# Optimization experiments

Hardware: AMD Instinct MI355X
Metric: run time of the kernel (lower is better)

## Reference

```python
import jax, jax.numpy as jnp
import numpy as np

B, T, C, H, S = 4, 1024, 768, 12, 64  # batch, seq, emb_dim, n_heads, head_size
FF = 4 * C          # 3072, ff_hidden_size (required by SwiGLU input dim)
HID = int(8 * C / 3)  # 2048, SwiGLU hidden
EPS = 1e-6


def _rope_tables(seq_len, dim):
    # theta = 10000 ** (-2 * arange(0, dim, 2) / dim)  (note extra factor 2 vs standard RoPE)
    theta = 10000.0 ** (-2.0 * jnp.arange(0, dim, 2, dtype=jnp.float32) / dim)
    freqs = jnp.arange(seq_len, dtype=jnp.float32)[:, None] * theta  # [T, dim/2]
    cos = jnp.repeat(jnp.cos(freqs), 2, axis=-1)  # [T, dim]
    sin = jnp.repeat(jnp.sin(freqs), 2, axis=-1)
    return cos, sin


def _rope(x, cos, sin):
    # x: [..., T, S]; rotate pairs: even' = -odd, odd' = even
    rot = jnp.stack([-x[..., 1::2], x[..., 0::2]], axis=-1).reshape(x.shape)
    return x * cos + rot * sin


def _rmsnorm(x, gamma):
    # global scalar RMS over the whole tensor (faithful to torch.mean with no dim)
    return x / jnp.sqrt(EPS + jnp.mean(x * x)) * gamma


def _block(x, Wq, Wk, Wv, Wo, g1, g2, W1, b1, Ww, bw, Wg, bg, Wd, bd, W2, b2):
    Tlen = x.shape[1]
    cos, sin = _rope_tables(Tlen, S)
    # --- multi-head attention on rms1(x) ---
    h = _rmsnorm(x, g1)
    q = jnp.einsum('btc,hcs->bhts', h, Wq)
    k = jnp.einsum('btc,hcs->bhts', h, Wk)
    v = jnp.einsum('btc,hcs->bhts', h, Wv)
    rq = _rope(q, cos, sin)
    rk = _rope(k, cos, sin)
    scores = jnp.einsum('bhts,bhks->bhtk', rq, rk) * (C ** -0.5)  # scale by emb_dim, faithful
    causal = jnp.tril(jnp.ones((Tlen, Tlen), dtype=bool))
    scores = jnp.where(causal, scores, -jnp.inf)
    probs = jax.nn.softmax(scores, axis=-1)
    attn = jnp.einsum('bhtk,bhks->bhts', probs, v)
    attn = attn.transpose(0, 2, 1, 3).reshape(x.shape[0], Tlen, C)  # concat heads
    out = x + attn @ Wo
    # --- feed forward on rms2(out) ---
    h2 = _rmsnorm(out, g2)
    u = h2 @ W1 + b1                      # [B,T,FF]
    wx = u @ Ww + bw                      # [B,T,HID]
    vx = u @ Wg + bg
    ff = (wx * (vx * jax.nn.sigmoid(vx))) @ Wd + bd  # [B,T,FF]
    ff = ff @ W2 + b2                     # [B,T,C]
    return out + ff


def setup_inputs() -> dict:
    key = jax.random.key(0)
    ks = jax.random.split(key, 17)
    sd = 0.02
    return {
        'x':  jax.random.normal(ks[0], (B, T, C), jnp.float32),
        'Wq': jax.random.normal(ks[1], (H, C, S), jnp.float32) * sd,
        'Wk': jax.random.normal(ks[2], (H, C, S), jnp.float32) * sd,
        'Wv': jax.random.normal(ks[3], (H, C, S), jnp.float32) * sd,
        'Wo': jax.random.normal(ks[4], (C, C), jnp.float32) * sd,
        'g1': jnp.ones((C,), jnp.float32),
        'g2': jnp.ones((C,), jnp.float32),
        'W1': jax.random.normal(ks[5], (C, FF), jnp.float32) * sd,
        'b1': jnp.zeros((FF,), jnp.float32),
        'Ww': jax.random.normal(ks[6], (FF, HID), jnp.float32) * sd,
        'bw': jnp.zeros((HID,), jnp.float32),
        'Wg': jax.random.normal(ks[7], (FF, HID), jnp.float32) * sd,
        'bg': jnp.zeros((HID,), jnp.float32),
        'Wd': jax.random.normal(ks[8], (HID, FF), jnp.float32) * sd,
        'bd': jnp.zeros((FF,), jnp.float32),
        'W2': jax.random.normal(ks[9], (FF, C), jnp.float32) * sd,
        'b2': jnp.zeros((C,), jnp.float32),
    }


def reference(x, Wq, Wk, Wv, Wo, g1, g2, W1, b1, Ww, bw, Wg, bg, Wd, bd, W2, b2):
    return _block(x, Wq, Wk, Wv, Wo, g1, g2, W1, b1, Ww, bw, Wg, bg, Wd, bd, W2, b2)
```

## Files before the change

kernel.cpp:

```cpp
#include <hip/hip_runtime.h>
#include <math.h>

#define BB   4
#define TT   1024
#define CC   768
#define HH   12
#define SS   64
#define FFD  3072
#define HIDD 2048
#define NTOK (BB*TT)
#define EPSR 1e-6f

typedef __attribute__((ext_vector_type(8))) short bf16x8;
typedef __attribute__((ext_vector_type(4))) float f32x4;

__device__ __forceinline__ unsigned short f2bf(float f) {
    unsigned u = __float_as_uint(f);
    return (unsigned short)((u + 0x7FFFu + ((u >> 16) & 1u)) >> 16);
}
__device__ __forceinline__ float bfl(unsigned u) { return __uint_as_float(u << 16); }
__device__ __forceinline__ float bfh(unsigned u) { return __uint_as_float(u & 0xFFFF0000u); }
__device__ __forceinline__ unsigned pk2(float a, float b) {
    return (unsigned)f2bf(a) | ((unsigned)f2bf(b) << 16);
}

__device__ __forceinline__ void gload_lds16(const unsigned short* g, unsigned short* l) {
    __builtin_amdgcn_global_load_lds(
        (const __attribute__((address_space(1))) unsigned int*)g,
        (__attribute__((address_space(3))) unsigned int*)l, 16, 0, 0);
}

__global__ void k_scale_gamma_b(const float* __restrict__ x, const float* __restrict__ g,
                                const float* __restrict__ part, unsigned short* __restrict__ h,
                                int n8, float invn, int npart) {
    __shared__ float sm[256];
    float s = 0.f;
    for (int i = threadIdx.x; i < npart; i += 256) s += part[i];
    sm[threadIdx.x] = s;
    __syncthreads();
    for (int off = 128; off > 0; off >>= 1) {
        if (threadIdx.x < off) sm[threadIdx.x] += sm[threadIdx.x + off];
        __syncthreads();
    }
    float sc = 1.0f / sqrtf(EPSR + sm[0] * invn);
    int i = blockIdx.x * blockDim.x + threadIdx.x;
    if (i >= n8) return;
    float4 v0 = ((const float4*)x)[2*i];
    float4 v1 = ((const float4*)x)[2*i+1];
    int c = (i * 8) % CC;
    float4 g0 = *(const float4*)(g + c);
    float4 g1v = *(const float4*)(g + c + 4);
    uint4 r;
    r.x = pk2(v0.x*sc*g0.x,  v0.y*sc*g0.y);
    r.y = pk2(v0.z*sc*g0.z,  v0.w*sc*g0.w);
    r.z = pk2(v1.x*sc*g1v.x, v1.y*sc*g1v.y);
    r.w = pk2(v1.z*sc*g1v.z, v1.w*sc*g1v.w);
    ((uint4*)h)[i] = r;
}

#define TQKV 1728
#define TWO  576
#define TW1  2304
#define TWW  6144
#define TWD  6144
#define TW2  2304
#define J0 (TQKV)
#define J1 (J0 + TWO)
#define J2 (J1 + TW1)
#define J3 (J2 + TWW)
#define J4 (J3 + TWW)
#define J5 (J4 + TWD)
#define J6 (J5 + TW2)
#define J7 (J6 + 16)
#define J8 (J7 + 128)
#define JSUM 1024
#define J9 (J8 + JSUM)

__device__ __forceinline__ void wT_tile(float (*tl)[33], const float* __restrict__ W,
                                        unsigned short* __restrict__ Wt,
                                        int K, int N, int t, int tx, int ty) {
    int nk = K >> 5;
    int k0 = (t % nk) * 32, n0 = (t / nk) * 32;
#pragma unroll
    for (int i = 0; i < 4; ++i)
        tl[ty + i*8][tx] = W[(size_t)(k0 + ty + i*8) * N + n0 + tx];
    __syncthreads();
#pragma unroll
    for (int i = 0; i < 4; ++i)
        Wt[(size_t)(n0 + ty + i*8) * K + k0 + tx] = f2bf(tl[tx][ty + i*8]);
}

__device__ __forceinline__ void wT_tile_il(float (*tl)[33], const float* __restrict__ W,
                                           unsigned short* __restrict__ Wt,
                                           int K, int N, int t, int tx, int ty, int ofs) {
    int nk = K >> 5;
    int k0 = (t % nk) * 32, n0 = (t / nk) * 32;
#pragma unroll
    for (int i = 0; i < 4; ++i)
        tl[ty + i*8][tx] = W[(size_t)(k0 + ty + i*8) * N + n0 + tx];
    __syncthreads();
#pragma unroll
    for (int i = 0; i < 4; ++i) {
        int j = n0 + ty + i*8;
        int pr = ((j & ~15) << 1) + ofs*16 + (j & 15);
        Wt[(size_t)pr * K + k0 + tx] = f2bf(tl[tx][ty + i*8]);
    }
}

__global__ void k_prep(const float* __restrict__ Wq, const float* __restrict__ Wk,
                       const float* __restrict__ Wv, const float* __restrict__ Wo,
                       const float* __restrict__ W1, const float* __restrict__ Ww,
                       const float* __restrict__ Wg, const float* __restrict__ Wd,
                       const float* __restrict__ W2, const float* __restrict__ bw,
                       const float* __restrict__ bg, const float* __restrict__ x,
                       unsigned short* __restrict__ wqkvT, unsigned short* __restrict__ WoT,
                       unsigned short* __restrict__ W1T, unsigned short* __restrict__ WcatT,
                       unsigned short* __restrict__ WdT, unsigned short* __restrict__ W2T,
                       float* __restrict__ bcat, float* __restrict__ tab,
                       float* __restrict__ part) {
    __shared__ float tl[32][33];
    const int bid = blockIdx.x;
    const int tx = threadIdx.x & 31, ty = threadIdx.x >> 5;
    if (bid < J0) {
        int t = bid;
        int c0 = (t % 24) * 32;
        int s0 = ((t / 24) & 1) * 32;
        int z = t / 48, sel = z / HH, h = z % HH;
        const float* W = (sel == 0 ? Wq : (sel == 1 ? Wk : Wv)) + (size_t)h * CC * SS;
#pragma unroll
        for (int i = 0; i < 4; ++i)
            tl[ty + i*8][tx] = W[(size_t)(c0 + ty + i*8) * SS + s0 + tx];
        __syncthreads();
#pragma unroll
        for (int i = 0; i < 4; ++i)
            wqkvT[(size_t)(sel*CC + h*SS + s0 + ty + i*8) * CC + c0 + tx] = f2bf(tl[tx][ty + i*8]);
    } else if (bid < J1) {
        wT_tile(tl, Wo, WoT, CC, CC, bid - J0, tx, ty);
    } else if (bid < J2) {
        wT_tile(tl, W1, W1T, CC, FFD, bid - J1, tx, ty);
    } else if (bid < J3) {
        wT_tile_il(tl, Ww, WcatT, FFD, HIDD, bid - J2, tx, ty, 0);
    } else if (bid < J4) {
        wT_tile_il(tl, Wg, WcatT, FFD, HIDD, bid - J3, tx, ty, 1);
    } else if (bid < J5) {
        wT_tile(tl, Wd, WdT, HIDD, FFD, bid - J4, tx, ty);
    } else if (bid < J6) {
        wT_tile(tl, W2, W2T, FFD, CC, bid - J5, tx, ty);
    } else if (bid < J7) {
        int ip = (bid - J6) * 256 + threadIdx.x;
        int lg = ((ip >> 5) << 4) + (ip & 15);
        bcat[ip] = ((ip >> 4) & 1) ? bg[lg] : bw[lg];
    } else if (bid < J8) {
        int i = (bid - J7) * 256 + threadIdx.x;
        int t = i >> 5, j = i & 31;
        float th = expf(-(float)j * 0.5756462732485115f);
        float ang = (float)t * th;
        tab[2*i]   = cosf(ang);
        tab[2*i+1] = sinf(ang);
    } else {
        float* sm = &tl[0][0];
        const int pb = bid - J8;
        const int n4 = NTOK * CC / 4;
        float s = 0.f;
        int stride = JSUM * 256;
        for (int i = pb * 256 + threadIdx.x; i < n4; i += stride) {
            float4 v = ((const float4*)x)[i];
            s += v.x*v.x + v.y*v.y + v.z*v.z + v.w*v.w;
        }
        sm[threadIdx.x] = s;
        __syncthreads();
        for (int off = 128; off > 0; off >>= 1) {
            if (threadIdx.x < off) sm[threadIdx.x] += sm[threadIdx.x + off];
            __syncthreads();
        }
        if (threadIdx.x == 0) part[pb] = sm[0];
    }
}

__global__ void k_rope_vt(unsigned short* __restrict__ qkv, const float* __restrict__ tab,
                          unsigned short* __restrict__ vtg) {
    const int bid = blockIdx.x;
    if (bid < 6144) {
        int i = bid * 256 + threadIdx.x;
        int j  = i & 31;
        int h  = (i >> 5) % HH;
        int bt = i / (32 * HH);
        int t  = bt & (TT - 1);
        float cs = tab[(t*32 + j)*2];
        float sn = tab[(t*32 + j)*2 + 1];
        size_t base = (size_t)bt * (3*CC) + h * SS + 2*j;
        unsigned q = *(unsigned*)(qkv + base);
        float qe = bfl(q), qo = bfh(q);
        *(unsigned*)(qkv + base) = pk2(qe*cs - qo*sn, qo*cs + qe*sn);
        unsigned k = *(unsigned*)(qkv + base + CC);
        float ke = bfl(k), ko = bfh(k);
        *(unsigned*)(qkv + base + CC) = pk2(ke*cs - ko*sn, ko*cs + ke*sn);
    } else {
        int b2 = bid - 6144;
        int bh = b2 >> 3, ty = b2 & 7;
        int b = bh / HH, h = bh % HH;
        int d = threadIdx.x & 63, tq = threadIdx.x >> 6;
        int t0 = ty * 128 + tq * 32;
        const unsigned short* src = qkv + (size_t)(b*TT + t0)*(3*CC) + 2*CC + h*SS + d;
        unsigned v[16];
#pragma unroll
        for (int e = 0; e < 16; ++e) {
            unsigned lo = src[(size_t)(2*e)*(3*CC)];
            unsigned hi = src[(size_t)(2*e+1)*(3*CC)];
            v[e] = (lo & 0xFFFFu) | (hi << 16);
        }
        uint4* dst = (uint4*)(vtg + ((size_t)bh*64 + d)*TT + t0);
#pragma unroll
        for (int q = 0; q < 4; ++q)
            dst[q] = make_uint4(v[q*4], v[q*4+1], v[q*4+2], v[q*4+3]);
    }
}

template<bool BIAS, bool RES, bool OUTB, bool SSQ>
__global__ __launch_bounds__(256) void k_gemm_bf16(
    const unsigned short* __restrict__ A, const unsigned short* __restrict__ Bt,
    const float* __restrict__ bias, const float* __restrict__ res,
    void* __restrict__ Cv, int M, int N, int K, float* __restrict__ ssq_part)
{
    __shared__ unsigned short As[2][128*32];
    __shared__ unsigned short Bs[2][128*32];
    __shared__ float smr[256];
    const int tid  = threadIdx.x;
    const int w    = tid >> 6, lane = tid & 63;
    const int wr   = w >> 1,  wc   = w & 1;
    const int row0 = blockIdx.y * 128, col0 = blockIdx.x * 128;

    f32x4 acc[4][4];
#pragma unroll
    for (int m = 0; m < 4; ++m)
#pragma unroll
        for (int n = 0; n < 4; ++n) acc[m][n] = (f32x4){0.f, 0.f, 0.f, 0.f};

    const int lr4 = lane >> 2;
    const int scb = lane & 3;

    auto stage = [&](int t, int buf) {
#pragma unroll
        for (int i = 0; i < 2; ++i) {
            int lr = w * 32 + i * 16 + lr4;
            int cbs = scb ^ ((lr >> 1) & 3);
            const unsigned short* ga = A + (size_t)(row0 + lr) * K + t * 32 + cbs * 8;
            gload_lds16(ga, &As[buf][(w * 32 + i * 16) * 32]);
            const unsigned short* gb = Bt + (size_t)(col0 + lr) * K + t * 32 + cbs * 8;
            gload_lds16(gb, &Bs[buf][(w * 32 + i * 16) * 32]);
        }
    };

    const int nt = K / 32;
    stage(0, 0);
    int cur = 0;
    const int fr = lane & 15, fq = lane >> 4;
    for (int t = 0; t < nt; ++t) {
        __syncthreads();
        if (t + 1 < nt) stage(t + 1, cur ^ 1);
        bf16x8 af[4], bf[4];
#pragma unroll
        for (int m = 0; m < 4; ++m) {
            int ra = wr * 64 + m * 16 + fr;
            af[m] = *(const bf16x8*)&As[cur][ra * 32 + (fq ^ ((ra >> 1) & 3)) * 8];
            int rb = wc * 64 + m * 16 + fr;
            bf[m] = *(const bf16x8*)&Bs[cur][rb * 32 + (fq ^ ((rb >> 1) & 3)) * 8];
        }
#pragma unroll
        for (int m = 0; m < 4; ++m)
#pragma unroll
            for (int n = 0; n < 4; ++n)
                acc[m][n] = __builtin_amdgcn_mfma_f32_16x16x32_bf16(af[m], bf[n], acc[m][n], 0, 0, 0);
        cur ^= 1;
    }

    float ssq = 0.f;
#pragma unroll
    for (int m = 0; m < 4; ++m) {
#pragma unroll
        for (int n = 0; n < 4; ++n) {
            int col = col0 + wc * 64 + n * 16 + fr;
            float bv = BIAS ? bias[col] : 0.f;
#pragma unroll
            for (int j = 0; j < 4; ++j) {
                int row = row0 + wr * 64 + m * 16 + fq * 4 + j;
                size_t off = (size_t)row * N + col;
                float v = acc[m][n][j] + bv;
                if (RES) v += res[off];
                if (OUTB) ((unsigned short*)Cv)[off] = f2bf(v);
                else      ((float*)Cv)[off] = v;
                if (SSQ) ssq += v * v;
            }
        }
    }
    if (SSQ) {
        smr[tid] = ssq;
        __syncthreads();
        for (int off = 128; off > 0; off >>= 1) {
            if (tid < off) smr[tid] += smr[tid + off];
            __syncthreads();
        }
        if (tid == 0) ssq_part[blockIdx.y * gridDim.x + blockIdx.x] = smr[0];
    }
}

#define GSTEP(s_, DOSTAGE, GATE)                                                  \
    {                                                                             \
        const int st_ = (s_) & 3;                                                 \
        const unsigned short* pa_ = &ringA[st_][0];                               \
        const unsigned short* pb_ = &ringB[st_][0];                               \
        bf16x8 af[8], bv[4];                                                      \
        _Pragma("unroll")                                                         \
        for (int m = 0; m < 8; ++m)                                               \
            af[m] = *(const bf16x8*)&pa_[offA[m]];                                \
        _Pragma("unroll")                                                         \
        for (int n = 0; n < 4; ++n)                                               \
            bv[n] = *(const bf16x8*)&pb_[offB[n]];                                \
        if (DOSTAGE) { stageA((s_) + 3); stageB((s_) + 3); }                      \
        __builtin_amdgcn_sched_barrier(0);                                        \
        __builtin_amdgcn_s_setprio(1);                                            \
        _Pragma("unroll")                                                         \
        for (int m = 0; m < 8; ++m)                                               \
            _Pragma("unroll")                                                     \
            for (int n = 0; n < 4; ++n)                                           \
                acc[m][n] = __builtin_amdgcn_mfma_f32_16x16x32_bf16(              \
                    af[m], bv[n], acc[m][n], 0, 0, 0);                            \
        __builtin_amdgcn_s_setprio(0);                                            \
        asm volatile("s_waitcnt " GATE ::: "memory");                             \
        __builtin_amdgcn_sched_barrier(0);                                        \
        __builtin_amdgcn_s_barrier();                                             \
    }

template<bool BIAS, bool SWIGLU>
__global__ __launch_bounds__(512, 2) void k_gemm256(
    const unsigned short* __restrict__ A, const unsigned short* __restrict__ Bt,
    const float* __restrict__ bias, unsigned short* __restrict__ C,
    int M, int N, int K)
{
    __shared__ __align__(16) unsigned short ringA[4][256*32];
    __shared__ __align__(16) unsigned short ringB[4][256*32];
    const int tid = threadIdx.x;
    const int w = tid >> 6, lane = tid & 63;
    const int wm = w >> 2, wn = w & 3;
    const int fr = lane & 15, fq = lane >> 4;

    const int nwg = gridDim.x * gridDim.y;
    const int bid = blockIdx.y * gridDim.x + blockIdx.x;
    const int cpx = nwg >> 3;
    const int sbid = (bid & 7) * cpx + (bid >> 3);
    const int row0 = (sbid / gridDim.x) * 256;
    const int col0 = (sbid % gridDim.x) * 256;

    f32x4 acc[8][4];
#pragma unroll
    for (int m = 0; m < 8; ++m)
#pragma unroll
        for (int n = 0; n < 4; ++n) acc[m][n] = (f32x4){0.f, 0.f, 0.f, 0.f};

    const int c0 = tid, c1 = 512 + tid;
    const int r0 = c0 >> 2, p0 = ((c0 & 3) ^ ((r0 >> 1) & 3)) * 8;
    const int r1 = c1 >> 2, p1 = ((c1 & 3) ^ ((r1 >> 1) & 3)) * 8;
    const unsigned short* aS0 = A  + (size_t)(row0 + r0) * K + p0;
    const unsigned short* aS1 = A  + (size_t)(row0 + r1) * K + p1;
    const unsigned short* bS0 = Bt + (size_t)(col0 + r0) * K + p0;
    const unsigned short* bS1 = Bt + (size_t)(col0 + r1) * K + p1;
    const int dL = w * 512;
    auto stageA = [&](int t) {
        const int st = t & 3;
        const int kb = t * 32;
        gload_lds16(aS0 + kb, &ringA[st][dL]);
        gload_lds16(aS1 + kb, &ringA[st][4096 + dL]);
    };
    auto stageB = [&](int t) {
        const int st = t & 3;
        const int kb = t * 32;
        gload_lds16(bS0 + kb, &ringB[st][dL]);
        gload_lds16(bS1 + kb, &ringB[st][4096 + dL]);
    };

    int offA[8], offB[4];
#pragma unroll
    for (int m = 0; m < 8; ++m) {
        int ra = wm*128 + m*16 + fr;
        offA[m] = ra*32 + (fq ^ ((ra >> 1) & 3))*8;
    }
#pragma unroll
    for (int n = 0; n < 4; ++n) {
        int rb = wn*64 + n*16 + fr;
        offB[n] = rb*32 + (fq ^ ((rb >> 1) & 3))*8;
    }

    const int S = K >> 5;
    stageA(0); stageB(0); stageA(1); stageB(1); stageA(2); stageB(2);
    asm volatile("s_waitcnt vmcnt(8)" ::: "memory");
    __builtin_amdgcn_s_barrier();
    int s = 0;
    for (; s < S - 3; ++s) GSTEP(s, true, "vmcnt(8)");
    GSTEP(s, false, "vmcnt(4)"); ++s;
    GSTEP(s, false, "vmcnt(0)"); ++s;
    GSTEP(s, false, "vmcnt(0)");

    if (SWIGLU) {
#pragma unroll
        for (int m = 0; m < 8; ++m) {
#pragma unroll
            for (int n = 0; n < 4; n += 2) {
                int colw = col0 + wn*64 + n*16 + fr;
                float bw_ = BIAS ? bias[colw] : 0.f;
                float bg_ = BIAS ? bias[colw + 16] : 0.f;
                int colo = ((colw >> 5) << 4) + (colw & 15);
#pragma unroll
                for (int j = 0; j < 4; ++j) {
                    int row = row0 + wm*128 + m*16 + fq*4 + j;
                    float wx = acc[m][n][j] + bw_;
                    float vx = acc[m][n+1][j] + bg_;
                    float sw = wx * vx / (1.f + __expf(-vx));
                    C[(size_t)row * (N >> 1) + colo] = f2bf(sw);
                }
            }
        }
    } else {
#pragma unroll
        for (int m = 0; m < 8; ++m) {
#pragma unroll
            for (int n = 0; n < 4; ++n) {
                int col = col0 + wn*64 + n*16 + fr;
                float bvb = BIAS ? bias[col] : 0.f;
#pragma unroll
                for (int j = 0; j < 4; ++j) {
                    int row = row0 + wm*128 + m*16 + fq*4 + j;
                    C[(size_t)row * N + col] = f2bf(acc[m][n][j] + bvb);
                }
            }
        }
    }
}

__global__ __launch_bounds__(256) void k_attn_mfma(
    const unsigned short* __restrict__ qkv, const unsigned short* __restrict__ vtg,
    unsigned short* __restrict__ attn)
{
    __shared__ __align__(16) unsigned short Ks[2][64*64];
    __shared__ __align__(16) unsigned short Vs[2][64*64];
    __shared__ __align__(16) unsigned short Ps[4][16*72];
    const int tid = threadIdx.x;
    const int w = tid >> 6, lane = tid & 63;
    const int fr = lane & 15, fq = lane >> 4;
    const int bh = blockIdx.x, b = bh / HH, h = bh % HH;
    const int qb = blockIdx.y * 64;
    const int nkt = qb / 64 + 1;
    const float scale = 0.03608439182435161f;

    bf16x8 qf[2];
    {
        const unsigned short* qp = qkv + (size_t)(b*TT + qb + w*16 + fr)*(3*CC) + h*SS + fq*8;
        qf[0] = *(const bf16x8*)qp;
        qf[1] = *(const bf16x8*)(qp + 32);
    }

    auto stage = [&](int kt, int buf) {
        const unsigned short* kbase = qkv + (size_t)(b*TT + kt*64)*(3*CC) + CC + h*SS;
        const unsigned short* vbase = vtg + ((size_t)bh*64)*TT + kt*64;
#pragma unroll
        for (int p = 0; p < 2; ++p) {
            int s = p*256 + tid;
            int row = s >> 3;
            int blk = (s & 7) ^ (row & 7);
            gload_lds16(kbase + (size_t)row*(3*CC) + blk*8, &Ks[buf][(p*256 + w*64)*8]);
            gload_lds16(vbase + (size_t)row*TT + blk*8,     &Vs[buf][(p*256 + w*64)*8]);
        }
    };

    float m[4] = {-INFINITY, -INFINITY, -INFINITY, -INFINITY};
    float l[4] = {0.f, 0.f, 0.f, 0.f};
    f32x4 oacc[4];
#pragma unroll
    for (int n = 0; n < 4; ++n) oacc[n] = (f32x4){0.f, 0.f, 0.f, 0.f};

    stage(0, 0);
    int cur = 0;
    for (int kt = 0; kt < nkt; ++kt) {
        __syncthreads();
        if (kt + 1 < nkt) stage(kt + 1, cur ^ 1);

        f32x4 sacc[4];
#pragma unroll
        for (int n = 0; n < 4; ++n) sacc[n] = (f32x4){0.f, 0.f, 0.f, 0.f};
#pragma unroll
        for (int ks = 0; ks < 2; ++ks) {
#pragma unroll
            for (int n = 0; n < 4; ++n) {
                int row = n*16 + fr;
                bf16x8 kf = *(const bf16x8*)&Ks[cur][row*64 + ((ks*4 + fq) ^ (row & 7))*8];
                sacc[n] = __builtin_amdgcn_mfma_f32_16x16x32_bf16(qf[ks], kf, sacc[n], 0, 0, 0);
            }
        }

        float sv[4][4];
        const bool lastt = (kt == nkt - 1);
        const int qloc = w*16 + fq*4;
#pragma unroll
        for (int n = 0; n < 4; ++n) {
            int kloc = n*16 + fr;
#pragma unroll
            for (int j = 0; j < 4; ++j) {
                float vv = sacc[n][j] * scale;
                if (lastt && kloc > qloc + j) vv = -INFINITY;
                sv[j][n] = vv;
            }
        }
        float mx[4], ls[4];
#pragma unroll
        for (int j = 0; j < 4; ++j)
            mx[j] = fmaxf(fmaxf(sv[j][0], sv[j][1]), fmaxf(sv[j][2], sv[j][3]));
#pragma unroll
        for (int d = 1; d < 16; d <<= 1)
#pragma unroll
            for (int j = 0; j < 4; ++j) mx[j] = fmaxf(mx[j], __shfl_xor(mx[j], d));
        float corr[4];
#pragma unroll
        for (int j = 0; j < 4; ++j) {
            float nm = fmaxf(m[j], mx[j]);
            corr[j] = __expf(m[j] - nm);
            m[j] = nm;
        }
#pragma unroll
        for (int j = 0; j < 4; ++j) {
            float s0 = 0.f;
#pragma unroll
            for (int n = 0; n < 4; ++n) {
                float p = __expf(sv[j][n] - m[j]);
                sv[j][n] = p;
                s0 += p;
            }
            ls[j] = s0;
        }
#pragma unroll
        for (int d = 1; d < 16; d <<= 1)
#pragma unroll
            for (int j = 0; j < 4; ++j) ls[j] += __shfl_xor(ls[j], d);
#pragma unroll
        for (int j = 0; j < 4; ++j) l[j] = l[j]*corr[j] + ls[j];
#pragma unroll
        for (int n = 0; n < 4; ++n)
#pragma unroll
            for (int j = 0; j < 4; ++j) oacc[n][j] *= corr[j];

#pragma unroll
        for (int j = 0; j < 4; ++j)
#pragma unroll
            for (int n = 0; n < 4; ++n)
                Ps[w][(fq*4 + j)*72 + n*16 + fr] = f2bf(sv[j][n]);

#pragma unroll
        for (int ks = 0; ks < 2; ++ks) {
            bf16x8 pf = *(const bf16x8*)&Ps[w][fr*72 + ks*32 + fq*8];
#pragma unroll
            for (int n = 0; n < 4; ++n) {
                int row = n*16 + fr;
                bf16x8 vf = *(const bf16x8*)&Vs[cur][row*64 + ((ks*4 + fq) ^ (row & 7))*8];
                oacc[n] = __builtin_amdgcn_mfma_f32_16x16x32_bf16(pf, vf, oacc[n], 0, 0, 0);
            }
        }
        cur ^= 1;
    }

    float inv[4];
#pragma unroll
    for (int j = 0; j < 4; ++j) inv[j] = 1.0f / l[j];
#pragma unroll
    for (int n = 0; n < 4; ++n)
#pragma unroll
        for (int j = 0; j < 4; ++j) {
            size_t off = (size_t)(b*TT + qb + w*16 + fq*4 + j)*CC + h*SS + n*16 + fr;
            attn[off] = f2bf(oacc[n][j] * inv[j]);
        }
}

extern "C" void kernel_launch(void* const* d_in, const int* in_sizes, int n_in,
                              void* d_out, int out_size, void* d_ws, size_t ws_size,
                              hipStream_t stream)
{
    const float* x  = (const float*)d_in[0];
    const float* Wq = (const float*)d_in[1];
    const float* Wk = (const float*)d_in[2];
    const float* Wv = (const float*)d_in[3];
    const float* Wo = (const float*)d_in[4];
    const float* g1 = (const float*)d_in[5];
    const float* g2 = (const float*)d_in[6];
    const float* W1 = (const float*)d_in[7];
    const float* b1 = (const float*)d_in[8];
    const float* Ww = (const float*)d_in[9];
    const float* bw = (const float*)d_in[10];
    const float* Wg = (const float*)d_in[11];
    const float* bg = (const float*)d_in[12];
    const float* Wd = (const float*)d_in[13];
    const float* bd = (const float*)d_in[14];
    const float* W2 = (const float*)d_in[15];
    const float* b2 = (const float*)d_in[16];
    float* out = (float*)d_out;

    char* p = (char*)d_ws;
    auto alloc = [&](size_t bytes) { char* r = p; p += (bytes + 255) & ~(size_t)255; return r; };

    float*          part   = (float*)alloc(4096);
    float*          tab    = (float*)alloc((size_t)TT*32*2*4);
    float*          bcat   = (float*)alloc((size_t)2*HIDD*4);
    unsigned short* hb     = (unsigned short*)alloc((size_t)NTOK*CC*2);
    unsigned short* wqkvT  = (unsigned short*)alloc((size_t)3*CC*CC*2);
    unsigned short* qkvb   = (unsigned short*)alloc((size_t)NTOK*3*CC*2);
    unsigned short* vtg    = (unsigned short*)alloc((size_t)BB*HH*SS*TT*2);
    unsigned short* attnb  = (unsigned short*)alloc((size_t)NTOK*CC*2);
    unsigned short* WoT    = (unsigned short*)alloc((size_t)CC*CC*2);
    unsigned short* W1T    = (unsigned short*)alloc((size_t)FFD*CC*2);
    unsigned short* ub     = (unsigned short*)alloc((size_t)NTOK*FFD*2);
    unsigned short* WcatT  = (unsigned short*)alloc((size_t)2*HIDD*FFD*2);
    unsigned short* swb    = (unsigned short*)alloc((size_t)NTOK*HIDD*2);
    unsigned short* WdT    = (unsigned short*)alloc((size_t)FFD*HIDD*2);
    unsigned short* W2T    = (unsigned short*)alloc((size_t)CC*FFD*2);

    const int n = NTOK * CC;

    k_prep<<<J9, 256, 0, stream>>>(Wq, Wk, Wv, Wo, W1, Ww, Wg, Wd, W2, bw, bg, x,
                                   wqkvT, WoT, W1T, WcatT, WdT, W2T, bcat, tab, part);

    k_scale_gamma_b<<<(n/8)/256, 256, 0, stream>>>(x, g1, part, hb, n/8,
                                                   1.0f/(float)n, JSUM);

    k_gemm256<false,false><<<dim3(3*CC/256, NTOK/256), 512, 0, stream>>>(
        hb, wqkvT, nullptr, qkvb, NTOK, 3*CC, CC);
    k_rope_vt<<<6144 + 384, 256, 0, stream>>>(qkvb, tab, vtg);

    k_attn_mfma<<<dim3(BB*HH, TT/64), 256, 0, stream>>>(qkvb, vtg, attnb);

    k_gemm_bf16<false,true,false,true><<<dim3(CC/128, NTOK/128), 256, 0, stream>>>(
        attnb, WoT, nullptr, x, out, NTOK, CC, CC, part);

    k_scale_gamma_b<<<(n/8)/256, 256, 0, stream>>>(out, g2, part, hb, n/8,
                                                   1.0f/(float)n, (CC/128)*(NTOK/128));

    k_gemm256<true,false><<<dim3(FFD/256, NTOK/256), 512, 0, stream>>>(
        hb, W1T, b1, ub, NTOK, FFD, CC);
    k_gemm256<true,true><<<dim3(2*HIDD/256, NTOK/256), 512, 0, stream>>>(
        ub, WcatT, bcat, swb, NTOK, 2*HIDD, FFD);
    k_gemm256<true,false><<<dim3(FFD/256, NTOK/256), 512, 0, stream>>>(
        swb, WdT, bd, ub, NTOK, FFD, HIDD);
    k_gemm_bf16<true,true,false,false><<<dim3(CC/128, NTOK/128), 256, 0, stream>>>(
        ub, W2T, b2, out, out, NTOK, CC, FFD, nullptr);
}
```

Measured before the change: 378.5 us.

## Fuse RoPE and V transpose into QKV GEMM epilogue via interleaved weight layout

Reorders the Q/K rows of the transposed QKV weight so that even and odd rotary pairs land in adjacent 16-column MFMA fragments. The QKV GEMM epilogue then applies RoPE in registers and writes V directly in transposed layout. This removes the separate rope/V-transpose kernel, along with its launch and its extra read and write pass over the QKV buffer. In exchange the epilogue becomes heavier, with table loads, 4-byte scattered stores, and strided writes into vtg.

Result: faster. 370.6 us (-2.1%).

```diff
diff --git a/kernel.cpp b/kernel.cpp
--- a/kernel.cpp
+++ b/kernel.cpp
@@ -132,8 +132,17 @@
             tl[ty + i*8][tx] = W[(size_t)(c0 + ty + i*8) * SS + s0 + tx];
         __syncthreads();
 #pragma unroll
-        for (int i = 0; i < 4; ++i)
-            wqkvT[(size_t)(sel*CC + h*SS + s0 + ty + i*8) * CC + c0 + tx] = f2bf(tl[tx][ty + i*8]);
+        for (int i = 0; i < 4; ++i) {
+            int s = s0 + ty + i*8;
+            int r;
+            if (sel < 2) {
+                int gp = h*32 + (s >> 1);
+                r = (gp >> 4)*32 + ((s & 1) << 4) + (gp & 15);
+            } else {
+                r = h*SS + s;
+            }
+            wqkvT[(size_t)(sel*CC + r) * CC + c0 + tx] = f2bf(tl[tx][ty + i*8]);
+        }
     } else if (bid < J1) {
         wT_tile(tl, Wo, WoT, CC, CC, bid - J0, tx, ty);
     } else if (bid < J2) {
@@ -177,45 +186,6 @@
     }
 }
 
-__global__ void k_rope_vt(unsigned short* __restrict__ qkv, const float* __restrict__ tab,
-                          unsigned short* __restrict__ vtg) {
-    const int bid = blockIdx.x;
-    if (bid < 6144) {
-        int i = bid * 256 + threadIdx.x;
-        int j  = i & 31;
-        int h  = (i >> 5) % HH;
-        int bt = i / (32 * HH);
-        int t  = bt & (TT - 1);
-        float cs = tab[(t*32 + j)*2];
-        float sn = tab[(t*32 + j)*2 + 1];
-        size_t base = (size_t)bt * (3*CC) + h * SS + 2*j;
-        unsigned q = *(unsigned*)(qkv + base);
-        float qe = bfl(q), qo = bfh(q);
-        *(unsigned*)(qkv + base) = pk2(qe*cs - qo*sn, qo*cs + qe*sn);
-        unsigned k = *(unsigned*)(qkv + base + CC);
-        float ke = bfl(k), ko = bfh(k);
-        *(unsigned*)(qkv + base + CC) = pk2(ke*cs - ko*sn, ko*cs + ke*sn);
-    } else {
-        int b2 = bid - 6144;
-        int bh = b2 >> 3, ty = b2 & 7;
-        int b = bh / HH, h = bh % HH;
-        int d = threadIdx.x & 63, tq = threadIdx.x >> 6;
-        int t0 = ty * 128 + tq * 32;
-        const unsigned short* src = qkv + (size_t)(b*TT + t0)*(3*CC) + 2*CC + h*SS + d;
-        unsigned v[16];
-#pragma unroll
-        for (int e = 0; e < 16; ++e) {
-            unsigned lo = src[(size_t)(2*e)*(3*CC)];
-            unsigned hi = src[(size_t)(2*e+1)*(3*CC)];
-            v[e] = (lo & 0xFFFFu) | (hi << 16);
-        }
-        uint4* dst = (uint4*)(vtg + ((size_t)bh*64 + d)*TT + t0);
-#pragma unroll
-        for (int q = 0; q < 4; ++q)
-            dst[q] = make_uint4(v[q*4], v[q*4+1], v[q*4+2], v[q*4+3]);
-    }
-}
-
 template<bool BIAS, bool RES, bool OUTB, bool SSQ>
 __global__ __launch_bounds__(256) void k_gemm_bf16(
     const unsigned short* __restrict__ A, const unsigned short* __restrict__ Bt,
@@ -331,11 +301,12 @@
         __builtin_amdgcn_s_barrier();                                             \
     }
 
-template<bool BIAS, bool SWIGLU>
+template<bool BIAS, bool SWIGLU, bool QKV>
 __global__ __launch_bounds__(512, 2) void k_gemm256(
     const unsigned short* __restrict__ A, const unsigned short* __restrict__ Bt,
     const float* __restrict__ bias, unsigned short* __restrict__ C,
-    int M, int N, int K)
+    int M, int N, int K, const float* __restrict__ tab,
+    unsigned short* __restrict__ vtg)
 {
     __shared__ __align__(16) unsigned short ringA[4][256*32];
     __shared__ __align__(16) unsigned short ringB[4][256*32];
@@ -400,7 +371,51 @@
     GSTEP(s, false, "vmcnt(0)"); ++s;
     GSTEP(s, false, "vmcnt(0)");
 
-    if (SWIGLU) {
+    if (QKV) {
+        if (col0 < 1536) {
+            const int sel = (col0 >= CC) ? 1 : 0;
+#pragma unroll
+            for (int m = 0; m < 8; ++m) {
+#pragma unroll
+                for (int np = 0; np < 2; ++np) {
+                    int colw = col0 + wn*64 + np*32 + fr;
+                    int ps = colw - sel*CC;
+                    int gp = (ps >> 5)*16 + (ps & 15);
+                    int hh = gp >> 5, jj = gp & 31;
+                    int ce = sel*CC + hh*64 + 2*jj;
+#pragma unroll
+                    for (int j = 0; j < 4; ++j) {
+                        int row = row0 + wm*128 + m*16 + fq*4 + j;
+                        int t = row & (TT - 1);
+                        float cs = tab[(t*32 + jj)*2];
+                        float sn = tab[(t*32 + jj)*2 + 1];
+                        float e = acc[m][2*np][j];
+                        float o = acc[m][2*np+1][j];
+                        *(unsigned*)(C + (size_t)row * N + ce) =
+                            pk2(e*cs - o*sn, o*cs + e*sn);
+                    }
+                }
+            }
+        } else {
+            const int vb = row0 >> 10;
+            const int tb = (row0 & (TT-1)) + wm*128;
+#pragma unroll
+            for (int m = 0; m < 8; ++m) {
+#pragma unroll
+                for (int n = 0; n < 4; ++n) {
+                    int col = col0 + wn*64 + n*16 + fr;
+                    int d = col - 1536;
+                    int t0 = tb + m*16 + fq*4;
+                    unsigned short* dst = vtg +
+                        ((size_t)(vb*HH + (d >> 6))*64 + (d & 63))*TT + t0;
+                    uint2 val;
+                    val.x = pk2(acc[m][n][0], acc[m][n][1]);
+                    val.y = pk2(acc[m][n][2], acc[m][n][3]);
+                    *(uint2*)dst = val;
+                }
+            }
+        }
+    } else if (SWIGLU) {
 #pragma unroll
         for (int m = 0; m < 8; ++m) {
 #pragma unroll
@@ -627,9 +642,8 @@
     k_scale_gamma_b<<<(n/8)/256, 256, 0, stream>>>(x, g1, part, hb, n/8,
                                                    1.0f/(float)n, JSUM);
 
-    k_gemm256<false,false><<<dim3(3*CC/256, NTOK/256), 512, 0, stream>>>(
-        hb, wqkvT, nullptr, qkvb, NTOK, 3*CC, CC);
-    k_rope_vt<<<6144 + 384, 256, 0, stream>>>(qkvb, tab, vtg);
+    k_gemm256<false,false,true><<<dim3(3*CC/256, NTOK/256), 512, 0, stream>>>(
+        hb, wqkvT, nullptr, qkvb, NTOK, 3*CC, CC, tab, vtg);
 
     k_attn_mfma<<<dim3(BB*HH, TT/64), 256, 0, stream>>>(qkvb, vtg, attnb);
 
@@ -639,12 +653,12 @@
     k_scale_gamma_b<<<(n/8)/256, 256, 0, stream>>>(out, g2, part, hb, n/8,
                                                    1.0f/(float)n, (CC/128)*(NTOK/128));
 
-    k_gemm256<true,false><<<dim3(FFD/256, NTOK/256), 512, 0, stream>>>(
-        hb, W1T, b1, ub, NTOK, FFD, CC);
-    k_gemm256<true,true><<<dim3(2*HIDD/256, NTOK/256), 512, 0, stream>>>(
-        ub, WcatT, bcat, swb, NTOK, 2*HIDD, FFD);
-    k_gemm256<true,false><<<dim3(FFD/256, NTOK/256), 512, 0, stream>>>(
-        swb, WdT, bd, ub, NTOK, FFD, HIDD);
+    k_gemm256<true,false,false><<<dim3(FFD/256, NTOK/256), 512, 0, stream>>>(
+        hb, W1T, b1, ub, NTOK, FFD, CC, nullptr, nullptr);
+    k_gemm256<true,true,false><<<dim3(2*HIDD/256, NTOK/256), 512, 0, stream>>>(
+        ub, WcatT, bcat, swb, NTOK, 2*HIDD, FFD, nullptr, nullptr);
+    k_gemm256<true,false,false><<<dim3(FFD/256, NTOK/256), 512, 0, stream>>>(
+        swb, WdT, bd, ub, NTOK, FFD, HIDD, nullptr, nullptr);
     k_gemm_bf16<true,true,false,false><<<dim3(CC/128, NTOK/128), 256, 0, stream>>>(
         ub, W2T, b2, out, out, NTOK, CC, FFD, nullptr);
 }
```
